# Optimization experiments

Measured on AMD Instinct MI355X. Metric: run time of the kernel, lower is better.

The kernel has to match this reference:

```python
import jax, jax.numpy as jnp
import numpy as np

B, T, D = 4, 2048, 1024
H = 16
HD = D // H  # 64

def setup_inputs() -> dict:
    key = jax.random.key(0)
    ks = jax.random.split(key, 7)
    s = 1.0 / np.sqrt(D)
    x = jax.random.normal(ks[0], (B, T, D), dtype=jnp.float32)
    # Per-head query projections stacked: Wq[h] maps D -> HD
    Wq = jax.random.uniform(ks[1], (H, D, HD), minval=-s, maxval=s, dtype=jnp.float32)
    bq = jax.random.uniform(ks[2], (H, HD), minval=-s, maxval=s, dtype=jnp.float32)
    Wk = jax.random.uniform(ks[3], (D, HD), minval=-s, maxval=s, dtype=jnp.float32)
    bk = jax.random.uniform(ks[4], (HD,), minval=-s, maxval=s, dtype=jnp.float32)
    Wv = jax.random.uniform(ks[5], (D, HD), minval=-s, maxval=s, dtype=jnp.float32)
    bv = jax.random.uniform(ks[6], (HD,), minval=-s, maxval=s, dtype=jnp.float32)
    return {"x": x, "Wq": Wq, "bq": bq, "Wk": Wk, "bk": bk, "Wv": Wv, "bv": bv}

def reference(x, Wq, bq, Wk, bk, Wv, bv):
    # shared single K/V head: [B, T, HD]
    k = jnp.einsum('btd,de->bte', x, Wk) + bk
    v = jnp.einsum('btd,de->bte', x, Wv) + bv
    # per-head queries batched: [B, H, T, HD]
    q = jnp.einsum('btd,hde->bhte', x, Wq) + bq[:, None, :]
    scale = 1.0 / jnp.sqrt(jnp.asarray(HD, dtype=x.dtype))
    scores = jnp.einsum('bhqe,bke->bhqk', q, k) * scale  # [B, H, T, T]
    attn = jax.nn.softmax(scores, axis=-1)
    out = jnp.einsum('bhqk,bke->bhqe', attn, v)  # [B, H, T, HD]
    # concat heads along last dim (head order matches torch cat order)
    return jnp.transpose(out, (0, 2, 1, 3)).reshape(B, T, H * HD)
```

## Files before the change

kernel.cpp:

```cpp
#include <hip/hip_runtime.h>

#define B 4
#define T 2048
#define D 1024
#define H 16
#define HD 64
#define NKT 32

typedef __attribute__((ext_vector_type(8))) short bf16x8;
typedef __attribute__((ext_vector_type(4))) float f32x4;
typedef __attribute__((ext_vector_type(16))) float f32x16;

#define MFMA16(a, b, c) __builtin_amdgcn_mfma_f32_16x16x32_bf16(a, b, c, 0, 0, 0)
#define MFMA32(a, b, c) __builtin_amdgcn_mfma_f32_32x32x16_bf16(a, b, c, 0, 0, 0)

static __device__ __forceinline__ unsigned short f2bf(float f) {
    union { float f; unsigned u; } v; v.f = f;
    unsigned r = v.u + 0x7FFFu + ((v.u >> 16) & 1u);
    return (unsigned short)(r >> 16);
}

static __device__ __forceinline__ bf16x8 cvt8(const float* p) {
    float4 a = *(const float4*)p;
    float4 b = *(const float4*)(p + 4);
    bf16x8 r;
    r[0] = (short)f2bf(a.x); r[1] = (short)f2bf(a.y);
    r[2] = (short)f2bf(a.z); r[3] = (short)f2bf(a.w);
    r[4] = (short)f2bf(b.x); r[5] = (short)f2bf(b.y);
    r[6] = (short)f2bf(b.z); r[7] = (short)f2bf(b.w);
    return r;
}

static __device__ __forceinline__ unsigned cvtpk(float lo, float hi) {
    unsigned r;
    asm("v_cvt_pk_bf16_f32 %0, %1, %2" : "=v"(r) : "v"(lo), "v"(hi));
    return r;
}

static __device__ __forceinline__ f32x16 zero16() {
    f32x16 z;
#pragma unroll
    for (int i = 0; i < 16; ++i) z[i] = 0.f;
    return z;
}

typedef __attribute__((address_space(1))) const unsigned char gl_u8;
typedef __attribute__((address_space(3))) unsigned char lds_u8;

static __device__ __forceinline__ void stage16(const void* g, void* l) {
    __builtin_amdgcn_global_load_lds((gl_u8*)(unsigned long long)g,
                                     (lds_u8*)(unsigned int)(unsigned long long)l,
                                     16, 0, 0);
}

__global__ __launch_bounds__(256) void cvt_x(const float* __restrict__ x,
                                             unsigned short* __restrict__ xbf) {
    int idx = (blockIdx.x * 256 + threadIdx.x) * 8;
    *(bf16x8*)(xbf + idx) = cvt8(x + idx);
}

__global__ __launch_bounds__(256) void pack_w(const float* __restrict__ Wq,
                                              const float* __restrict__ Wk,
                                              const float* __restrict__ Wv,
                                              unsigned short* __restrict__ Wqt,
                                              unsigned short* __restrict__ Wkt,
                                              unsigned short* __restrict__ Wvt) {
    __shared__ float tile[64][65];
    int hh = blockIdx.x >> 4, db = blockIdx.x & 15;
    const float* src;
    unsigned short* dst;
    if (hh < 16)      { src = Wq + (size_t)hh * D * HD; dst = Wqt + (size_t)hh * HD * D; }
    else if (hh == 16){ src = Wk; dst = Wkt; }
    else              { src = Wv; dst = Wvt; }
    int r = threadIdx.x >> 6, c = threadIdx.x & 63;
    int d0 = db * 64;
#pragma unroll
    for (int i = 0; i < 16; ++i)
        tile[r * 16 + i][c] = src[(size_t)(d0 + r * 16 + i) * HD + c];
    __syncthreads();
#pragma unroll
    for (int j = 0; j < 16; ++j)
        dst[(size_t)(r * 16 + j) * D + d0 + c] = f2bf(tile[c][r * 16 + j]);
}

__global__ __launch_bounds__(256) void kv_gemm(const unsigned short* __restrict__ xbf,
                                               const unsigned short* __restrict__ Wkt,
                                               const unsigned short* __restrict__ Wvt,
                                               const float* __restrict__ bk,
                                               const float* __restrict__ bv,
                                               unsigned char* __restrict__ Ksw,
                                               unsigned char* __restrict__ Vsw) {
    int grp = blockIdx.x >> 7;
    int rtb = blockIdx.x & 127;
    int wave = threadIdx.x >> 6;
    int lane = threadIdx.x & 63;
    int ln = lane & 15, lk = lane >> 4;
    int rt = rtb * 4 + wave;
    int t0 = rt * 16;

    const unsigned short* Wt = grp ? Wvt : Wkt;
    const float* bias = grp ? bv : bk;

    f32x4 acc[4];
#pragma unroll
    for (int e = 0; e < 4; ++e) acc[e] = (f32x4){0.f, 0.f, 0.f, 0.f};

    for (int d0 = 0; d0 < D; d0 += 32) {
        bf16x8 a = *(const bf16x8*)(xbf + (size_t)(t0 + ln) * D + d0 + lk * 8);
#pragma unroll
        for (int e = 0; e < 4; ++e) {
            bf16x8 w = *(const bf16x8*)(Wt + (size_t)(e * 16 + ln) * D + d0 + lk * 8);
            acc[e] = MFMA16(a, w, acc[e]);
        }
    }

#pragma unroll
    for (int e = 0; e < 4; ++e)
#pragma unroll
        for (int r = 0; r < 4; ++r) {
            int trow = t0 + lk * 4 + r;
            int ecol = e * 16 + ln;
            float val = acc[e][r] + bias[ecol];
            int bb = trow >> 11, tl = trow & 2047;
            int ktile = tl >> 6;
            size_t tbase = ((size_t)(bb * NKT + ktile)) << 13;
            if (grp == 0) {
                int rr = tl & 63, cb = 2 * ecol;
                *(unsigned short*)(Ksw + tbase + rr * 128 + (cb ^ ((rr & 7) << 4))) = f2bf(val);
            } else {
                int ko = tl & 63, cb = 2 * ko;
                *(unsigned short*)(Vsw + tbase + ecol * 128 + (cb ^ ((ecol & 7) << 4))) = f2bf(val);
            }
        }
}

__global__ __launch_bounds__(256, 4) void attn(const unsigned short* __restrict__ xbf,
                                               const unsigned short* __restrict__ Wqt,
                                               const float* __restrict__ bq,
                                               const unsigned char* __restrict__ Ksw,
                                               const unsigned char* __restrict__ Vsw,
                                               float* __restrict__ out) {
    __shared__ __align__(16) unsigned char smem[33280];

    int blk = ((blockIdx.x & 7) << 7) | (blockIdx.x >> 3);
    int qt = blk & 15;
    int h  = (blk >> 4) & 15;
    int b  = blk >> 8;
    int wave = threadIdx.x >> 6, lane = threadIdx.x & 63;
    int l31 = lane & 31, hi = lane >> 5;
    int t0 = qt * 128 + wave * 32;

    const unsigned char* Kt = Ksw + (((size_t)b * NKT) << 13);
    const unsigned char* Vt = Vsw + (((size_t)b * NKT) << 13);
    int soff = wave * 1024 + lane * 16;
    int ldsw = wave * 1024;

    auto STAGE = [&](int kt, int lk, int lv) {
        const unsigned char* gK = Kt + ((size_t)kt << 13);
        const unsigned char* gV = Vt + ((size_t)kt << 13);
        stage16(gK + soff,        smem + lk + ldsw);
        stage16(gK + 4096 + soff, smem + lk + 4096 + ldsw);
        stage16(gV + soff,        smem + lv + ldsw);
        stage16(gV + 4096 + soff, smem + lv + 4096 + ldsw);
    };

    STAGE(0, 0, 16384);

    f32x16 qacc[2] = {zero16(), zero16()};
    const unsigned short* Wh = Wqt + (size_t)h * HD * D;
    const unsigned short* xrow  = xbf + (size_t)(b * T + t0 + l31) * D + hi * 8;
    const unsigned short* wrow0 = Wh + (size_t)l31 * D + hi * 8;
    const unsigned short* wrow1 = Wh + (size_t)(32 + l31) * D + hi * 8;
    for (int dk = 0; dk < D; dk += 16) {
        bf16x8 xb = *(const bf16x8*)(xrow + dk);
        qacc[0] = MFMA32(*(const bf16x8*)(wrow0 + dk), xb, qacc[0]);
        qacc[1] = MFMA32(*(const bf16x8*)(wrow1 + dk), xb, qacc[1]);
    }

    const float sl2 = 0.125f * 1.44269504f;
    float qv[2][16];
#pragma unroll
    for (int e0 = 0; e0 < 2; ++e0)
#pragma unroll
        for (int r = 0; r < 16; ++r) {
            int crow = (r & 3) + 8 * (r >> 2) + 4 * hi;
            qv[e0][r] = (qacc[e0][r] + bq[h * HD + e0 * 32 + crow]) * sl2;
        }

    bf16x8 qf[4];
#pragma unroll
    for (int dt = 0; dt < 4; ++dt) {
        int s = dt >> 1;
        int b0 = 8 * (dt & 1), b1 = b0 + 4;
        unsigned c0 = cvtpk(qv[s][b0 + 0], qv[s][b0 + 1]);
        unsigned c1 = cvtpk(qv[s][b0 + 2], qv[s][b0 + 3]);
        unsigned c2 = cvtpk(qv[s][b1 + 0], qv[s][b1 + 1]);
        unsigned c3 = cvtpk(qv[s][b1 + 2], qv[s][b1 + 3]);
        auto r02 = __builtin_amdgcn_permlane32_swap(c0, c2, false, false);
        auto r13 = __builtin_amdgcn_permlane32_swap(c1, c3, false, false);
        union { unsigned u[4]; bf16x8 v; } pu;
        pu.u[0] = r02[0]; pu.u[1] = r13[0]; pu.u[2] = r02[1]; pu.u[3] = r13[1];
        qf[dt] = pu.v;
    }

    const unsigned char* bp[4];
    int sw = (l31 & 7) << 4;
#pragma unroll
    for (int dt = 0; dt < 4; ++dt)
        bp[dt] = smem + l31 * 128 + ((dt * 32 + hi * 16) ^ sw);

    __syncthreads();

    float mrun = -1e30f, lrun = 0.f;
    f32x16 o[2] = {zero16(), zero16()};

    auto TILE = [&](int cur, int ck, int cv, int nxt, int nk, int nv) {
        if (nxt < NKT) STAGE(nxt, nk, nv);

        f32x16 sacc[2] = {zero16(), zero16()};
        __builtin_amdgcn_s_setprio(1);
#pragma unroll
        for (int dt = 0; dt < 4; ++dt) {
            bf16x8 kf0 = *(const bf16x8*)(bp[dt] + ck);
            bf16x8 kf1 = *(const bf16x8*)(bp[dt] + ck + 4096);
            sacc[0] = MFMA32(kf0, qf[dt], sacc[0]);
            sacc[1] = MFMA32(kf1, qf[dt], sacc[1]);
        }
        __builtin_amdgcn_s_setprio(0);

        float mx[8];
#pragma unroll
        for (int i = 0; i < 8; ++i)
            mx[i] = fmaxf(fmaxf(sacc[0][i], sacc[0][i + 8]),
                          fmaxf(sacc[1][i], sacc[1][i + 8]));
#pragma unroll
        for (int i = 0; i < 4; ++i) mx[i] = fmaxf(mx[i], mx[i + 4]);
        float pmax = fmaxf(fmaxf(mx[0], mx[1]), fmaxf(mx[2], mx[3]));
        pmax = fmaxf(pmax, __shfl_xor(pmax, 32));

        if (__any(pmax - mrun > 8.0f)) {
            float newm = fmaxf(mrun, pmax);
            float corr = exp2f(mrun - newm);
            mrun = newm;
            lrun *= corr;
#pragma unroll
            for (int e0 = 0; e0 < 2; ++e0)
#pragma unroll
                for (int r = 0; r < 16; ++r) o[e0][r] *= corr;
        }

#pragma unroll
        for (int kt2 = 0; kt2 < 2; ++kt2)
#pragma unroll
            for (int r = 0; r < 16; ++r)
                sacc[kt2][r] = exp2f(sacc[kt2][r] - mrun);

        float sm[8];
#pragma unroll
        for (int i = 0; i < 8; ++i)
            sm[i] = (sacc[0][i] + sacc[0][i + 8]) + (sacc[1][i] + sacc[1][i + 8]);
#pragma unroll
        for (int i = 0; i < 4; ++i) sm[i] += sm[i + 4];
        float rsum = (sm[0] + sm[1]) + (sm[2] + sm[3]);
        rsum += __shfl_xor(rsum, 32);
        lrun += rsum;

        __builtin_amdgcn_s_setprio(1);
#pragma unroll
        for (int ks = 0; ks < 4; ++ks) {
            int s = ks >> 1;
            int b0 = 8 * (ks & 1), b1 = b0 + 4;
            bf16x8 vf0 = *(const bf16x8*)(bp[ks] + cv);
            bf16x8 vf1 = *(const bf16x8*)(bp[ks] + cv + 4096);
            unsigned c0 = cvtpk(sacc[s][b0 + 0], sacc[s][b0 + 1]);
            unsigned c1 = cvtpk(sacc[s][b0 + 2], sacc[s][b0 + 3]);
            unsigned c2 = cvtpk(sacc[s][b1 + 0], sacc[s][b1 + 1]);
            unsigned c3 = cvtpk(sacc[s][b1 + 2], sacc[s][b1 + 3]);
            auto r02 = __builtin_amdgcn_permlane32_swap(c0, c2, false, false);
            auto r13 = __builtin_amdgcn_permlane32_swap(c1, c3, false, false);
            union { unsigned u[4]; bf16x8 v; } pu;
            pu.u[0] = r02[0]; pu.u[1] = r13[0]; pu.u[2] = r02[1]; pu.u[3] = r13[1];
            o[0] = MFMA32(vf0, pu.v, o[0]);
            o[1] = MFMA32(vf1, pu.v, o[1]);
        }
        __builtin_amdgcn_s_setprio(0);

        __syncthreads();
    };

    for (int kt = 0; kt < NKT; kt += 2) {
        TILE(kt,     0,    16384, kt + 1, 8192, 24576);
        TILE(kt + 1, 8192, 24576, kt + 2, 0,    16384);
    }

    float inv = 1.f / lrun;
    float (*lds_t)[32][65] = (float (*)[32][65])smem;
#pragma unroll
    for (int e0 = 0; e0 < 2; ++e0)
#pragma unroll
        for (int r = 0; r < 16; ++r) {
            int crow = (r & 3) + 8 * (r >> 2) + 4 * hi;
            lds_t[wave][l31][e0 * 32 + crow] = o[e0][r] * inv;
        }
    __syncthreads();

    int rgrp = lane >> 4;
    int cg = (lane & 15) * 4;
#pragma unroll
    for (int g = 0; g < 8; ++g) {
        int row = g * 4 + rgrp;
        float4 vv;
        vv.x = lds_t[wave][row][cg + 0];
        vv.y = lds_t[wave][row][cg + 1];
        vv.z = lds_t[wave][row][cg + 2];
        vv.w = lds_t[wave][row][cg + 3];
        *(float4*)(out + (size_t)(b * T + t0 + row) * D + h * HD + cg) = vv;
    }
}

extern "C" void kernel_launch(void* const* d_in, const int* in_sizes, int n_in,
                              void* d_out, int out_size, void* d_ws, size_t ws_size,
                              hipStream_t stream) {
    const float* x  = (const float*)d_in[0];
    const float* Wq = (const float*)d_in[1];
    const float* bq = (const float*)d_in[2];
    const float* Wk = (const float*)d_in[3];
    const float* bk = (const float*)d_in[4];
    const float* Wv = (const float*)d_in[5];
    const float* bv = (const float*)d_in[6];
    float* out = (float*)d_out;

    unsigned char* ws = (unsigned char*)d_ws;
    unsigned short* xbf = (unsigned short*)(ws);
    unsigned short* Wqt = (unsigned short*)(ws + 16777216);
    unsigned short* Wkt = (unsigned short*)(ws + 18874368);
    unsigned short* Wvt = (unsigned short*)(ws + 19005440);
    unsigned char*  Ksw = ws + 19136512;
    unsigned char*  Vsw = ws + 20185088;

    cvt_x<<<4096, 256, 0, stream>>>(x, xbf);
    pack_w<<<288, 256, 0, stream>>>(Wq, Wk, Wv, Wqt, Wkt, Wvt);
    kv_gemm<<<256, 256, 0, stream>>>(xbf, Wkt, Wvt, bk, bv, Ksw, Vsw);
    attn<<<1024, 256, 0, stream>>>(xbf, Wqt, bq, Ksw, Vsw, out);
}
```

Measured before the change: 207.4 us.

## Fuse x conversion into KV GEMM and pre-layout K/V fragments for linear LDS reads

Removes the standalone cvt_x kernel: kv_gemm now converts fp32 x to bf16 on the fly and writes xbf as a side product for the attention kernel. K and V are written in a fragment-ordered layout, so attention reads MFMA operands with lane-linear 16-byte LDS loads, and all V fragments are loaded before the softmax. Cross-half reductions use permlane32_swap instead of shfl_xor, and the epilogue transpose uses an XOR-swizzled buffer with float4 reads. Trade-offs: more V registers stay live per tile, and the KV GEMM now also does the conversion and the extra xbf writes.

```diff
diff --git a/kernel.cpp b/kernel.cpp
--- a/kernel.cpp
+++ b/kernel.cpp
@@ -44,6 +44,17 @@
     return z;
 }
 
+static __device__ __forceinline__ float xhalf_max(float x) {
+    unsigned u = __float_as_uint(x);
+    auto r = __builtin_amdgcn_permlane32_swap(u, u, false, false);
+    return fmaxf(__uint_as_float(r[0]), __uint_as_float(r[1]));
+}
+static __device__ __forceinline__ float xhalf_sum(float x) {
+    unsigned u = __float_as_uint(x);
+    auto r = __builtin_amdgcn_permlane32_swap(u, u, false, false);
+    return __uint_as_float(r[0]) + __uint_as_float(r[1]);
+}
+
 typedef __attribute__((address_space(1))) const unsigned char gl_u8;
 typedef __attribute__((address_space(3))) unsigned char lds_u8;
 
@@ -51,12 +62,6 @@
     __builtin_amdgcn_global_load_lds((gl_u8*)(unsigned long long)g,
                                      (lds_u8*)(unsigned int)(unsigned long long)l,
                                      16, 0, 0);
-}
-
-__global__ __launch_bounds__(256) void cvt_x(const float* __restrict__ x,
-                                             unsigned short* __restrict__ xbf) {
-    int idx = (blockIdx.x * 256 + threadIdx.x) * 8;
-    *(bf16x8*)(xbf + idx) = cvt8(x + idx);
 }
 
 __global__ __launch_bounds__(256) void pack_w(const float* __restrict__ Wq,
@@ -83,11 +88,12 @@
         dst[(size_t)(r * 16 + j) * D + d0 + c] = f2bf(tile[c][r * 16 + j]);
 }
 
-__global__ __launch_bounds__(256) void kv_gemm(const unsigned short* __restrict__ xbf,
+__global__ __launch_bounds__(256) void kv_gemm(const float* __restrict__ xf,
                                                const unsigned short* __restrict__ Wkt,
                                                const unsigned short* __restrict__ Wvt,
                                                const float* __restrict__ bk,
                                                const float* __restrict__ bv,
+                                               unsigned short* __restrict__ xbf,
                                                unsigned char* __restrict__ Ksw,
                                                unsigned char* __restrict__ Vsw) {
     int grp = blockIdx.x >> 7;
@@ -106,7 +112,9 @@
     for (int e = 0; e < 4; ++e) acc[e] = (f32x4){0.f, 0.f, 0.f, 0.f};
 
     for (int d0 = 0; d0 < D; d0 += 32) {
-        bf16x8 a = *(const bf16x8*)(xbf + (size_t)(t0 + ln) * D + d0 + lk * 8);
+        size_t xi = (size_t)(t0 + ln) * D + d0 + lk * 8;
+        bf16x8 a = cvt8(xf + xi);
+        if (grp == 0) *(bf16x8*)(xbf + xi) = a;
 #pragma unroll
         for (int e = 0; e < 4; ++e) {
             bf16x8 w = *(const bf16x8*)(Wt + (size_t)(e * 16 + ln) * D + d0 + lk * 8);
@@ -119,17 +127,19 @@
 #pragma unroll
         for (int r = 0; r < 4; ++r) {
             int trow = t0 + lk * 4 + r;
-            int ecol = e * 16 + ln;
-            float val = acc[e][r] + bias[ecol];
+            float val = acc[e][r] + bias[e * 16 + ln];
             int bb = trow >> 11, tl = trow & 2047;
-            int ktile = tl >> 6;
-            size_t tbase = ((size_t)(bb * NKT + ktile)) << 13;
+            size_t tbase = ((size_t)(bb * NKT + (tl >> 6))) << 13;
+            int key = tl & 63;
             if (grp == 0) {
-                int rr = tl & 63, cb = 2 * ecol;
-                *(unsigned short*)(Ksw + tbase + rr * 128 + (cb ^ ((rr & 7) << 4))) = f2bf(val);
+                int off = (e * 2 + (key >> 5)) * 1024 +
+                          ((ln >> 3) * 32 + (key & 31)) * 16 + (ln & 7) * 2;
+                *(unsigned short*)(Ksw + tbase + off) = f2bf(val);
             } else {
-                int ko = tl & 63, cb = 2 * ko;
-                *(unsigned short*)(Vsw + tbase + ecol * 128 + (cb ^ ((ecol & 7) << 4))) = f2bf(val);
+                int off = ((key >> 4) * 2 + (e >> 1)) * 1024 +
+                          (((key >> 3) & 1) * 32 + (e & 1) * 16 + ln) * 16 +
+                          (key & 7) * 2;
+                *(unsigned short*)(Vsw + tbase + off) = f2bf(val);
             }
         }
 }
@@ -140,7 +150,7 @@
                                                const unsigned char* __restrict__ Ksw,
                                                const unsigned char* __restrict__ Vsw,
                                                float* __restrict__ out) {
-    __shared__ __align__(16) unsigned char smem[33280];
+    __shared__ __align__(16) unsigned char smem[32768];
 
     int blk = ((blockIdx.x & 7) << 7) | (blockIdx.x >> 3);
     int qt = blk & 15;
@@ -203,30 +213,31 @@
         qf[dt] = pu.v;
     }
 
-    const unsigned char* bp[4];
-    int sw = (l31 & 7) << 4;
-#pragma unroll
-    for (int dt = 0; dt < 4; ++dt)
-        bp[dt] = smem + l31 * 128 + ((dt * 32 + hi * 16) ^ sw);
+    const unsigned char* fbase = smem + lane * 16;
 
     __syncthreads();
 
     float mrun = -1e30f, lrun = 0.f;
     f32x16 o[2] = {zero16(), zero16()};
 
-    auto TILE = [&](int cur, int ck, int cv, int nxt, int nk, int nv) {
+    auto TILE = [&](int ck, int cv, int nxt, int nk, int nv) {
         if (nxt < NKT) STAGE(nxt, nk, nv);
 
         f32x16 sacc[2] = {zero16(), zero16()};
         __builtin_amdgcn_s_setprio(1);
 #pragma unroll
         for (int dt = 0; dt < 4; ++dt) {
-            bf16x8 kf0 = *(const bf16x8*)(bp[dt] + ck);
-            bf16x8 kf1 = *(const bf16x8*)(bp[dt] + ck + 4096);
+            bf16x8 kf0 = *(const bf16x8*)(fbase + ck + (dt * 2 + 0) * 1024);
+            bf16x8 kf1 = *(const bf16x8*)(fbase + ck + (dt * 2 + 1) * 1024);
             sacc[0] = MFMA32(kf0, qf[dt], sacc[0]);
             sacc[1] = MFMA32(kf1, qf[dt], sacc[1]);
         }
         __builtin_amdgcn_s_setprio(0);
+
+        bf16x8 vfa[8];
+#pragma unroll
+        for (int c = 0; c < 8; ++c)
+            vfa[c] = *(const bf16x8*)(fbase + cv + c * 1024);
 
         float mx[8];
 #pragma unroll
@@ -236,7 +247,7 @@
 #pragma unroll
         for (int i = 0; i < 4; ++i) mx[i] = fmaxf(mx[i], mx[i + 4]);
         float pmax = fmaxf(fmaxf(mx[0], mx[1]), fmaxf(mx[2], mx[3]));
-        pmax = fmaxf(pmax, __shfl_xor(pmax, 32));
+        pmax = xhalf_max(pmax);
 
         if (__any(pmax - mrun > 8.0f)) {
             float newm = fmaxf(mrun, pmax);
@@ -262,16 +273,13 @@
 #pragma unroll
         for (int i = 0; i < 4; ++i) sm[i] += sm[i + 4];
         float rsum = (sm[0] + sm[1]) + (sm[2] + sm[3]);
-        rsum += __shfl_xor(rsum, 32);
-        lrun += rsum;
+        lrun += xhalf_sum(rsum);
 
         __builtin_amdgcn_s_setprio(1);
 #pragma unroll
         for (int ks = 0; ks < 4; ++ks) {
             int s = ks >> 1;
             int b0 = 8 * (ks & 1), b1 = b0 + 4;
-            bf16x8 vf0 = *(const bf16x8*)(bp[ks] + cv);
-            bf16x8 vf1 = *(const bf16x8*)(bp[ks] + cv + 4096);
             unsigned c0 = cvtpk(sacc[s][b0 + 0], sacc[s][b0 + 1]);
             unsigned c1 = cvtpk(sacc[s][b0 + 2], sacc[s][b0 + 3]);
             unsigned c2 = cvtpk(sacc[s][b1 + 0], sacc[s][b1 + 1]);
@@ -280,8 +288,8 @@
             auto r13 = __builtin_amdgcn_permlane32_swap(c1, c3, false, false);
             union { unsigned u[4]; bf16x8 v; } pu;
             pu.u[0] = r02[0]; pu.u[1] = r13[0]; pu.u[2] = r02[1]; pu.u[3] = r13[1];
-            o[0] = MFMA32(vf0, pu.v, o[0]);
-            o[1] = MFMA32(vf1, pu.v, o[1]);
+            o[0] = MFMA32(vfa[ks * 2 + 0], pu.v, o[0]);
+            o[1] = MFMA32(vfa[ks * 2 + 1], pu.v, o[1]);
         }
         __builtin_amdgcn_s_setprio(0);
 
@@ -289,32 +297,29 @@
     };
 
     for (int kt = 0; kt < NKT; kt += 2) {
-        TILE(kt,     0,    16384, kt + 1, 8192, 24576);
-        TILE(kt + 1, 8192, 24576, kt + 2, 0,    16384);
+        TILE(0,    16384, kt + 1, 8192, 24576);
+        TILE(8192, 24576, kt + 2, 0,    16384);
     }
 
     float inv = 1.f / lrun;
-    float (*lds_t)[32][65] = (float (*)[32][65])smem;
+    unsigned char* eb = smem + wave * 8192;
 #pragma unroll
     for (int e0 = 0; e0 < 2; ++e0)
 #pragma unroll
         for (int r = 0; r < 16; ++r) {
             int crow = (r & 3) + 8 * (r >> 2) + 4 * hi;
-            lds_t[wave][l31][e0 * 32 + crow] = o[e0][r] * inv;
+            int col4 = (e0 * 32 + crow) * 4;
+            *(float*)(eb + l31 * 256 + (col4 ^ ((l31 & 15) << 4))) = o[e0][r] * inv;
         }
     __syncthreads();
 
     int rgrp = lane >> 4;
-    int cg = (lane & 15) * 4;
+    int c16 = (lane & 15) * 16;
 #pragma unroll
     for (int g = 0; g < 8; ++g) {
         int row = g * 4 + rgrp;
-        float4 vv;
-        vv.x = lds_t[wave][row][cg + 0];
-        vv.y = lds_t[wave][row][cg + 1];
-        vv.z = lds_t[wave][row][cg + 2];
-        vv.w = lds_t[wave][row][cg + 3];
-        *(float4*)(out + (size_t)(b * T + t0 + row) * D + h * HD + cg) = vv;
+        float4 vv = *(const float4*)(eb + row * 256 + (c16 ^ ((row & 15) << 4)));
+        *(float4*)(out + (size_t)(b * T + t0 + row) * D + h * HD + (c16 >> 2)) = vv;
     }
 }
 
@@ -338,8 +343,7 @@
     unsigned char*  Ksw = ws + 19136512;
     unsigned char*  Vsw = ws + 20185088;
 
-    cvt_x<<<4096, 256, 0, stream>>>(x, xbf);
     pack_w<<<288, 256, 0, stream>>>(Wq, Wk, Wv, Wqt, Wkt, Wvt);
-    kv_gemm<<<256, 256, 0, stream>>>(xbf, Wkt, Wvt, bk, bv, Ksw, Vsw);
+    kv_gemm<<<256, 256, 0, stream>>>(x, Wkt, Wvt, bk, bv, xbf, Ksw, Vsw);
     attn<<<1024, 256, 0, stream>>>(xbf, Wqt, bq, Ksw, Vsw, out);
 }
```

Measured after the change: 216.4 us. 4.3% more time.
